# Kernel optimization log

Hardware: AMD Instinct MI355X
Metric: run time of the kernel (lower is better)

The kernel has to match this reference:

```python
import jax, jax.numpy as jnp
import numpy as np

N = 50000      # nodes
E = 800000     # edges (before self-loops)
H = 4          # heads
C = 64         # hidden_unit per head
IN = 256       # input_dim
OUT = 64       # output_dim
NEG = 0.2      # LeakyReLU slope in GATConv
EPS = 1e-5     # BatchNorm eps


def setup_inputs() -> dict:
    key = jax.random.key(0)
    ks = jax.random.split(key, 12)
    s = 0.05
    HC = H * C
    return {
        'x': jax.random.normal(ks[0], (N, IN), dtype=jnp.float32),
        'edge_index': jax.random.randint(ks[1], (2, E), 0, N, dtype=jnp.int64),
        # GATConv layer 1
        'W1': jax.random.normal(ks[2], (IN, HC), dtype=jnp.float32) * s,
        'att_src1': jax.random.normal(ks[3], (H, C), dtype=jnp.float32) * s,
        'att_dst1': jax.random.normal(ks[4], (H, C), dtype=jnp.float32) * s,
        'b1': jnp.zeros((HC,), jnp.float32),
        # GATConv layer 2
        'W2': jax.random.normal(ks[5], (HC, HC), dtype=jnp.float32) * s,
        'att_src2': jax.random.normal(ks[6], (H, C), dtype=jnp.float32) * s,
        'att_dst2': jax.random.normal(ks[7], (H, C), dtype=jnp.float32) * s,
        'b2': jnp.zeros((HC,), jnp.float32),
        # BatchNorms
        'g1': jnp.ones((HC,), jnp.float32), 'beta1': jnp.zeros((HC,), jnp.float32),
        'g2': jnp.ones((HC,), jnp.float32), 'beta2': jnp.zeros((HC,), jnp.float32),
        # final Linear
        'Wl': jax.random.normal(ks[8], (HC, OUT), dtype=jnp.float32) * s,
        'bl': jnp.zeros((OUT,), jnp.float32),
    }


def gat_layer(x, src, dst, W, a_src, a_dst, b):
    # x: [N, F_in] -> per-head features [N, H, C]
    xh = (x @ W).reshape(-1, H, C)
    alpha_src = jnp.einsum('nhc,hc->nh', xh, a_src)   # [N, H]
    alpha_dst = jnp.einsum('nhc,hc->nh', xh, a_dst)   # [N, H]
    e = jax.nn.leaky_relu(alpha_src[src] + alpha_dst[dst], NEG)  # [Etot, H]
    # segment softmax over edges grouped by destination node
    m = jax.ops.segment_max(e, dst, num_segments=N)              # [N, H]
    ex = jnp.exp(e - m[dst])
    den = jax.ops.segment_sum(ex, dst, num_segments=N)           # [N, H]
    alpha = ex / (den[dst] + 1e-16)                              # [Etot, H]
    # weighted scatter-add aggregation
    out = jax.ops.segment_sum(alpha[:, :, None] * xh[src], dst, num_segments=N)
    return out.reshape(-1, H * C) + b


def batchnorm(x, g, beta):
    mu = x.mean(axis=0)
    var = x.var(axis=0)
    return (x - mu) * jax.lax.rsqrt(var + EPS) * g + beta


def reference(x, edge_index, W1, att_src1, att_dst1, b1,
              W2, att_src2, att_dst2, b2, g1, beta1, g2, beta2, Wl, bl):
    # GATConv adds self-loops by default
    loops = jnp.arange(N, dtype=edge_index.dtype)
    src = jnp.concatenate([edge_index[0], loops])
    dst = jnp.concatenate([edge_index[1], loops])
    h = batchnorm(gat_layer(x, src, dst, W1, att_src1, att_dst1, b1), g1, beta1)
    # dropout is identity in eval mode
    h = batchnorm(gat_layer(h, src, dst, W2, att_src2, att_dst2, b2), g2, beta2)
    emb = h @ Wl + bl
    out = jax.nn.log_softmax(emb, axis=1)
    return (out, emb)
```

## Files before the change

### kernel.cpp

```cpp
#include <hip/hip_runtime.h>
#include <cstdint>

#define NNODES 50000
#define NEDGES 800000
#define ETOT   (NEDGES + NNODES)
#define HEADS 4
#define CH 64
#define HC 256
#define INDIM 256
#define OUTDIM 64
#define NEG_SLOPE 0.2f
#define BN_EPS 1e-5f
#define NB 128

typedef unsigned short u16;
typedef unsigned int u32;
typedef __attribute__((ext_vector_type(8))) short short8;
typedef __attribute__((ext_vector_type(8))) unsigned short ushort8v;
typedef __attribute__((ext_vector_type(4))) float floatx4;

__device__ inline float bf2f(u16 u) {
    union { unsigned int i; float f; } c;
    c.i = ((unsigned int)u) << 16;
    return c.f;
}
__device__ inline u16 f2bf(float f) {
    union { float f; unsigned int i; } c;
    c.f = f;
    unsigned int u = c.i + 0x7fff + ((c.i >> 16) & 1);
    return (u16)(u >> 16);
}
__device__ __host__ inline int pos256(int b) {
    int h = b >> 6, c = b & 63;
    return h * 64 + (c & 15) * 4 + (c >> 4);
}
__device__ inline void async16(u16* lds, const u16* g) {
    __builtin_amdgcn_global_load_lds(
        (const __attribute__((address_space(1))) unsigned int*)g,
        (__attribute__((address_space(3))) unsigned int*)lds,
        16, 0, 0);
}


__global__ void hist_kernel(const int* __restrict__ ei, int* __restrict__ cnt) {
    int t = blockIdx.x * blockDim.x + threadIdx.x;
    if (t >= ETOT) return;
    int d = (t < NEDGES) ? ei[NEDGES + t] : (t - NEDGES);
    atomicAdd(&cnt[d], 1);
}

__global__ void scan1_kernel(const int* __restrict__ cnt, int* __restrict__ row_off,
                             int* __restrict__ blockSums) {
    __shared__ int tsum[256];
    const int tid = threadIdx.x;
    const int base = blockIdx.x * 4096 + tid * 16;
    int local[16];
    int run = 0;
#pragma unroll
    for (int i = 0; i < 16; ++i) {
        int idx = base + i;
        int v = (idx < NNODES) ? cnt[idx] : 0;
        local[i] = run;
        run += v;
    }
    tsum[tid] = run;
    __syncthreads();
    for (int d = 1; d < 256; d <<= 1) {
        int v = (tid >= d) ? tsum[tid - d] : 0;
        __syncthreads();
        tsum[tid] += v;
        __syncthreads();
    }
    int excl = (tid == 0) ? 0 : tsum[tid - 1];
#pragma unroll
    for (int i = 0; i < 16; ++i) {
        int idx = base + i;
        if (idx < NNODES) row_off[idx] = excl + local[i];
    }
    if (tid == 0) blockSums[blockIdx.x] = tsum[255];
}

__global__ void scan2_kernel(int* __restrict__ row_off, const int* __restrict__ blockSums,
                             int* __restrict__ nxt) {
    __shared__ int sprefix;
    if (threadIdx.x == 0) {
        int p = 0;
        for (int b = 0; b < (int)blockIdx.x; ++b) p += blockSums[b];
        sprefix = p;
    }
    __syncthreads();
    int prefix = sprefix;
    int base = blockIdx.x * 4096 + threadIdx.x * 16;
#pragma unroll
    for (int i = 0; i < 16; ++i) {
        int idx = base + i;
        if (idx < NNODES) {
            int v = row_off[idx] + prefix;
            row_off[idx] = v;
            nxt[idx] = v;
        }
    }
    if (blockIdx.x == 0 && threadIdx.x == 0) row_off[NNODES] = ETOT;
}

__global__ void fill_csr_kernel(const int* __restrict__ ei, int* __restrict__ nxt,
                                int2* __restrict__ csr_pair) {
    int t = blockIdx.x * blockDim.x + threadIdx.x;
    if (t >= ETOT) return;
    int s, d;
    if (t < NEDGES) { s = ei[t]; d = ei[NEDGES + t]; }
    else            { s = d = t - NEDGES; }
    int pos = atomicAdd(&nxt[d], 1);
    csr_pair[pos] = make_int2(s, d);
}


__global__ void wcast_kernel(const float* __restrict__ W, u16* __restrict__ Wt,
                             int K, int Ncols) {
    int t = blockIdx.x * blockDim.x + threadIdx.x;
    if (t >= K * Ncols) return;
    int k = t / Ncols, n = t - k * Ncols;
    Wt[n * K + k] = f2bf(W[t]);
}


template <bool AF32>
__global__ __launch_bounds__(256)
void gemm_gat_kernel(const void* __restrict__ Ap, const u16* __restrict__ Bt,
                     const float* __restrict__ bias,
                     const float* __restrict__ att_s, const float* __restrict__ att_d,
                     u16* __restrict__ xhp, float* __restrict__ asrc,
                     float* __restrict__ adst, int M, int K) {
    __shared__ u16 As[128 * 32];
    __shared__ u16 Bs[128 * 32];
    const int tid = threadIdx.x;
    const int wave = tid >> 6, lane = tid & 63;
    const int q15 = lane & 15, quad = lane >> 4;
    const int rowBase = blockIdx.y * 128;
    const int colBase = blockIdx.x * 128;
    const int waveM = (wave >> 1) * 64, waveN = (wave & 1) * 64;
    const int head = blockIdx.x * 2 + (wave & 1);

    floatx4 acc[4][4];
    floatx4 zero = {0.f, 0.f, 0.f, 0.f};
#pragma unroll
    for (int i = 0; i < 4; ++i)
#pragma unroll
        for (int j = 0; j < 4; ++j) acc[i][j] = zero;

    for (int kt = 0; kt < K; kt += 32) {
        if constexpr (AF32) {
            const float* A32 = (const float*)Ap;
#pragma unroll
            for (int rnd = 0; rnd < 4; ++rnd) {
                int slot = rnd * 256 + tid;
                int r = slot >> 3, c4 = (slot & 7) * 4;
                int ar = rowBase + r; if (ar >= M) ar = M - 1;
                float4 fv = *(const float4*)&A32[(size_t)ar * K + kt + c4];
                ushort4 o;
                o.x = f2bf(fv.x); o.y = f2bf(fv.y); o.z = f2bf(fv.z); o.w = f2bf(fv.w);
                *(ushort4*)&As[r * 32 + c4] = o;
            }
#pragma unroll
            for (int q = 0; q < 2; ++q) {
                int e8 = (wave * 2 + q) * 64 + lane;
                int r = e8 >> 2, c = (e8 & 3) * 8;
                async16(&Bs[(wave * 2 + q) * 512], &Bt[(size_t)(colBase + r) * K + kt + c]);
            }
        } else {
            const u16* A16 = (const u16*)Ap;
#pragma unroll
            for (int q = 0; q < 2; ++q) {
                int e8 = (wave * 2 + q) * 64 + lane;
                int r = e8 >> 2, c = (e8 & 3) * 8;
                int ar = rowBase + r; if (ar >= M) ar = M - 1;
                async16(&As[(wave * 2 + q) * 512], &A16[(size_t)ar * K + kt + c]);
                async16(&Bs[(wave * 2 + q) * 512], &Bt[(size_t)(colBase + r) * K + kt + c]);
            }
        }
        __syncthreads();

        short8 af[4], bfr[4];
#pragma unroll
        for (int i = 0; i < 4; ++i)
            af[i] = *(const short8*)&As[(waveM + i * 16 + q15) * 32 + quad * 8];
#pragma unroll
        for (int j = 0; j < 4; ++j)
            bfr[j] = *(const short8*)&Bs[(waveN + j * 16 + q15) * 32 + quad * 8];
#pragma unroll
        for (int i = 0; i < 4; ++i)
#pragma unroll
            for (int j = 0; j < 4; ++j)
                acc[i][j] = __builtin_amdgcn_mfma_f32_16x16x32_bf16(af[i], bfr[j], acc[i][j], 0, 0, 0);
        __syncthreads();
    }

    float bv[4], atsv[4], atdv[4];
#pragma unroll
    for (int j = 0; j < 4; ++j) {
        int gcol = colBase + waveN + j * 16 + q15;
        bv[j] = bias ? bias[gcol] : 0.f;
        int hc = head * CH + j * 16 + q15;
        atsv[j] = att_s[hc];
        atdv[j] = att_d[hc];
    }
    const int pbase = head * 64 + q15 * 4;

#pragma unroll
    for (int i = 0; i < 4; ++i) {
#pragma unroll
        for (int rr = 0; rr < 4; ++rr) {
            int grow = rowBase + waveM + i * 16 + quad * 4 + rr;
            float v[4];
#pragma unroll
            for (int j = 0; j < 4; ++j) v[j] = acc[i][j][rr] + bv[j];
            float s = v[0] * atsv[0] + v[1] * atsv[1] + v[2] * atsv[2] + v[3] * atsv[3];
            float d = v[0] * atdv[0] + v[1] * atdv[1] + v[2] * atdv[2] + v[3] * atdv[3];
#pragma unroll
            for (int off = 1; off <= 8; off <<= 1) {
                s += __shfl_xor(s, off, 64);
                d += __shfl_xor(d, off, 64);
            }
            ushort4 o;
            o.x = f2bf(v[0]); o.y = f2bf(v[1]); o.z = f2bf(v[2]); o.w = f2bf(v[3]);
            if (grow < M) {
                *(ushort4*)&xhp[(size_t)grow * HC + pbase] = o;
                if (q15 == 0) {
                    asrc[grow * 4 + head] = s;
                    adst[grow * 4 + head] = d;
                }
            }
        }
    }
}


__global__ void wedge_kernel(const int2* __restrict__ csr_pair,
                             const float* __restrict__ asrc, const float* __restrict__ adst,
                             u16* __restrict__ w4b) {
    int e = blockIdx.x * blockDim.x + threadIdx.x;
    if (e >= ETOT) return;
    int2 pr = csr_pair[e];
    float4 a = *(const float4*)&asrc[pr.x * 4];
    float4 b = *(const float4*)&adst[pr.y * 4];
    ushort4 r;
    float v;
    v = a.x + b.x; v = v > 0.f ? v : NEG_SLOPE * v; r.x = f2bf(__expf(v));
    v = a.y + b.y; v = v > 0.f ? v : NEG_SLOPE * v; r.y = f2bf(__expf(v));
    v = a.z + b.z; v = v > 0.f ? v : NEG_SLOPE * v; r.z = f2bf(__expf(v));
    v = a.w + b.w; v = v > 0.f ? v : NEG_SLOPE * v; r.w = f2bf(__expf(v));
    *(ushort4*)&w4b[(size_t)e * 4] = r;
}


__global__ __launch_bounds__(256)
void aggregate_kernel(const int* __restrict__ row_off, const int2* __restrict__ csr_pair,
                      const u16* __restrict__ w4b, const u16* __restrict__ xhp,
                      const float* __restrict__ bias, u16* __restrict__ out) {
    const int g = threadIdx.x >> 6;
    const int lane = threadIdx.x & 63;
    const int d = blockIdx.x * 4 + g;
    const int h = lane >> 4;
    const int c16 = lane & 15;
    const int poff = h * 64 + c16 * 4;
    const int hsel = h & 2;
    const int hsh = (h & 1) * 16;
    const int start = row_off[d], end = row_off[d + 1];
    float a0 = 0.f, a1 = 0.f, a2 = 0.f, a3 = 0.f, den = 0.f;

    for (int base = start; base < end; base += 64) {
        const int cnt = min(64, end - base);
        int sv = 0;
        u32 wx = 0, wy = 0;
        if (lane < cnt) {
            int e = base + lane;
            sv = csr_pair[e].x;
            uint2 wq = *(const uint2*)&w4b[(size_t)e * 4];
            wx = wq.x; wy = wq.y;
        }
        int k = 0;
        for (; k + 3 < cnt; k += 4) {
            int s0 = __builtin_amdgcn_readlane(sv, k);
            int s1 = __builtin_amdgcn_readlane(sv, k + 1);
            int s2 = __builtin_amdgcn_readlane(sv, k + 2);
            int s3 = __builtin_amdgcn_readlane(sv, k + 3);
            u32 x0w = __builtin_amdgcn_readlane((int)wx, k), y0w = __builtin_amdgcn_readlane((int)wy, k);
            u32 x1w = __builtin_amdgcn_readlane((int)wx, k + 1), y1w = __builtin_amdgcn_readlane((int)wy, k + 1);
            u32 x2w = __builtin_amdgcn_readlane((int)wx, k + 2), y2w = __builtin_amdgcn_readlane((int)wy, k + 2);
            u32 x3w = __builtin_amdgcn_readlane((int)wx, k + 3), y3w = __builtin_amdgcn_readlane((int)wy, k + 3);
            ushort4 v0 = *(const ushort4*)&xhp[(size_t)s0 * HC + poff];
            ushort4 v1 = *(const ushort4*)&xhp[(size_t)s1 * HC + poff];
            ushort4 v2 = *(const ushort4*)&xhp[(size_t)s2 * HC + poff];
            ushort4 v3 = *(const ushort4*)&xhp[(size_t)s3 * HC + poff];
            float w0 = bf2f((u16)((hsel ? y0w : x0w) >> hsh));
            float w1 = bf2f((u16)((hsel ? y1w : x1w) >> hsh));
            float w2 = bf2f((u16)((hsel ? y2w : x2w) >> hsh));
            float w3 = bf2f((u16)((hsel ? y3w : x3w) >> hsh));
            den += (w0 + w1) + (w2 + w3);
            a0 += w0 * bf2f(v0.x) + w1 * bf2f(v1.x) + w2 * bf2f(v2.x) + w3 * bf2f(v3.x);
            a1 += w0 * bf2f(v0.y) + w1 * bf2f(v1.y) + w2 * bf2f(v2.y) + w3 * bf2f(v3.y);
            a2 += w0 * bf2f(v0.z) + w1 * bf2f(v1.z) + w2 * bf2f(v2.z) + w3 * bf2f(v3.z);
            a3 += w0 * bf2f(v0.w) + w1 * bf2f(v1.w) + w2 * bf2f(v2.w) + w3 * bf2f(v3.w);
        }
        for (; k < cnt; ++k) {
            int s0 = __builtin_amdgcn_readlane(sv, k);
            u32 x0w = __builtin_amdgcn_readlane((int)wx, k), y0w = __builtin_amdgcn_readlane((int)wy, k);
            ushort4 v0 = *(const ushort4*)&xhp[(size_t)s0 * HC + poff];
            float w0 = bf2f((u16)((hsel ? y0w : x0w) >> hsh));
            den += w0;
            a0 += w0 * bf2f(v0.x);
            a1 += w0 * bf2f(v0.y);
            a2 += w0 * bf2f(v0.z);
            a3 += w0 * bf2f(v0.w);
        }
    }
    float inv = 1.f / (den + 1e-16f);
    const int ch0 = h * 64 + c16;
    ushort4 o;
    o.x = f2bf(a0 * inv + bias[ch0 +  0]);
    o.y = f2bf(a1 * inv + bias[ch0 + 16]);
    o.z = f2bf(a2 * inv + bias[ch0 + 32]);
    o.w = f2bf(a3 * inv + bias[ch0 + 48]);
    *(ushort4*)&out[(size_t)d * HC + poff] = o;
}


__global__ __launch_bounds__(256)
void bn_stats_kernel(const u16* __restrict__ x, float* __restrict__ part) {
    const int tid = threadIdx.x;
    float s[8] = {}, s2[8] = {};
    const size_t total = (size_t)NNODES * HC;
    const size_t stride = (size_t)NB * 256 * 8;
    for (size_t f = ((size_t)blockIdx.x * 256 + tid) * 8; f < total; f += stride) {
        ushort8v v = *(const ushort8v*)&x[f];
#pragma unroll
        for (int i = 0; i < 8; ++i) {
            float t = bf2f(v[i]);
            s[i] += t;
            s2[i] += t * t;
        }
    }
#pragma unroll
    for (int i = 0; i < 8; ++i) {
        s[i] += __shfl_xor(s[i], 32, 64);
        s2[i] += __shfl_xor(s2[i], 32, 64);
    }
    __shared__ float red[4][512];
    const int wave = tid >> 6, lane = tid & 63;
    if (lane < 32) {
#pragma unroll
        for (int i = 0; i < 8; ++i) {
            red[wave][lane * 8 + i] = s[i];
            red[wave][256 + lane * 8 + i] = s2[i];
        }
    }
    __syncthreads();
    for (int j = tid; j < 512; j += 256)
        part[(size_t)blockIdx.x * 512 + j] = red[0][j] + red[1][j] + red[2][j] + red[3][j];
}


__global__ __launch_bounds__(256)
void fold_kernel(const float* __restrict__ W, const float* __restrict__ part,
                 const float* __restrict__ g, const float* __restrict__ beta,
                 const float* __restrict__ baseBias,
                 u16* __restrict__ Wt, float* __restrict__ biasOut, int Ncols) {
    __shared__ float sh[256];
    __shared__ float stat2[2];
    const int b = blockIdx.x;
    const int tid = threadIdx.x;
    if (b < 256) {
        const int p = pos256(b);
        const int wave = tid >> 6, lane = tid & 63;
        if (wave < 2) {
            int off = wave * 256;
            float v = part[(size_t)lane * 512 + off + p] + part[(size_t)(lane + 64) * 512 + off + p];
#pragma unroll
            for (int o = 1; o <= 32; o <<= 1) v += __shfl_xor(v, o, 64);
            if (lane == 0) stat2[wave] = v;
        }
        __syncthreads();
        float mu = stat2[0] * (1.f / NNODES);
        float var = stat2[1] * (1.f / NNODES) - mu * mu;
        float rg = rsqrtf(var + BN_EPS) * g[b];
        for (int n = tid; n < Ncols; n += 256)
            Wt[n * 256 + p] = f2bf(W[b * Ncols + n] * rg);
    } else {
        const int p = pos256(tid);
        float sum = 0.f, sq = 0.f;
        for (int k = 0; k < NB; ++k) {
            sum += part[(size_t)k * 512 + p];
            sq += part[(size_t)k * 512 + 256 + p];
        }
        float mu = sum * (1.f / NNODES);
        float var = sq * (1.f / NNODES) - mu * mu;
        float rg = rsqrtf(var + BN_EPS) * g[tid];
        sh[tid] = beta[tid] - mu * rg;
        __syncthreads();
        if (tid < Ncols) {
            float acc = baseBias ? baseBias[tid] : 0.f;
            for (int k = 0; k < 256; ++k) acc += sh[k] * W[k * Ncols + tid];
            biasOut[tid] = acc;
        }
    }
}


__global__ __launch_bounds__(256)
void final_ls_kernel(const u16* __restrict__ A, const u16* __restrict__ Bt,
                     const float* __restrict__ bias,
                     float* __restrict__ emb, float* __restrict__ out, int M) {
    __shared__ u16 As[128 * 32];
    __shared__ u16 Bs[64 * 32];
    const int tid = threadIdx.x;
    const int wave = tid >> 6, lane = tid & 63;
    const int q15 = lane & 15, quad = lane >> 4;
    const int rowBase = blockIdx.x * 128;

    floatx4 acc[2][4];
    floatx4 zero = {0.f, 0.f, 0.f, 0.f};
#pragma unroll
    for (int i = 0; i < 2; ++i)
#pragma unroll
        for (int j = 0; j < 4; ++j) acc[i][j] = zero;

    for (int kt = 0; kt < 256; kt += 32) {
#pragma unroll
        for (int rnd = 0; rnd < 2; ++rnd) {
            int slot = rnd * 256 + wave * 64 + lane;
            int r = slot >> 2;
            int c = (slot & 3) * 8;
            int ar = rowBase + r; if (ar >= M) ar = M - 1;
            async16(&As[(rnd * 256 + wave * 64) * 8], &A[(size_t)ar * 256 + kt + c]);
        }
        {
            int slot = wave * 64 + lane;
            int r = slot >> 2;
            int c = (slot & 3) * 8;
            async16(&Bs[(wave * 64) * 8], &Bt[(size_t)r * 256 + kt + c]);
        }
        __syncthreads();

        short8 af[2], bfr[4];
#pragma unroll
        for (int i = 0; i < 2; ++i)
            af[i] = *(const short8*)&As[(wave * 32 + i * 16 + q15) * 32 + quad * 8];
#pragma unroll
        for (int j = 0; j < 4; ++j)
            bfr[j] = *(const short8*)&Bs[(j * 16 + q15) * 32 + quad * 8];
#pragma unroll
        for (int i = 0; i < 2; ++i)
#pragma unroll
            for (int j = 0; j < 4; ++j)
                acc[i][j] = __builtin_amdgcn_mfma_f32_16x16x32_bf16(af[i], bfr[j], acc[i][j], 0, 0, 0);
        __syncthreads();
    }

#pragma unroll
    for (int i = 0; i < 2; ++i) {
#pragma unroll
        for (int rr = 0; rr < 4; ++rr) {
            float v[4];
#pragma unroll
            for (int j = 0; j < 4; ++j) v[j] = acc[i][j][rr] + bias[j * 16 + q15];
            float m = fmaxf(fmaxf(v[0], v[1]), fmaxf(v[2], v[3]));
#pragma unroll
            for (int off = 1; off <= 8; off <<= 1) m = fmaxf(m, __shfl_xor(m, off, 64));
            float s = __expf(v[0] - m) + __expf(v[1] - m) + __expf(v[2] - m) + __expf(v[3] - m);
#pragma unroll
            for (int off = 1; off <= 8; off <<= 1) s += __shfl_xor(s, off, 64);
            float ls = m + logf(s);
            int grow = rowBase + wave * 32 + i * 16 + quad * 4 + rr;
            if (grow < M) {
#pragma unroll
                for (int j = 0; j < 4; ++j) {
                    int col = j * 16 + q15;
                    emb[(size_t)grow * OUTDIM + col] = v[j];
                    out[(size_t)grow * OUTDIM + col] = v[j] - ls;
                }
            }
        }
    }
}


extern "C" void kernel_launch(void* const* d_in, const int* in_sizes, int n_in,
                              void* d_out, int out_size, void* d_ws, size_t ws_size,
                              hipStream_t stream) {
    const float* x   = (const float*)d_in[0];
    const int*   ei  = (const int*)d_in[1];
    const float* W1  = (const float*)d_in[2];
    const float* at_s1 = (const float*)d_in[3];
    const float* at_d1 = (const float*)d_in[4];
    const float* b1  = (const float*)d_in[5];
    const float* W2  = (const float*)d_in[6];
    const float* at_s2 = (const float*)d_in[7];
    const float* at_d2 = (const float*)d_in[8];
    const float* b2  = (const float*)d_in[9];
    const float* g1  = (const float*)d_in[10];
    const float* be1 = (const float*)d_in[11];
    const float* g2  = (const float*)d_in[12];
    const float* be2 = (const float*)d_in[13];
    const float* Wl  = (const float*)d_in[14];
    const float* bl  = (const float*)d_in[15];

    float* out = (float*)d_out;
    float* emb = out + (size_t)NNODES * OUTDIM;

    char* ws = (char*)d_ws;
    size_t off = 0;
    auto alloc = [&](size_t bytes) {
        void* p = ws + off;
        off += (bytes + 255) & ~(size_t)255;
        return p;
    };
    int*   cnt     = (int*)alloc((size_t)NNODES * 4);
    int*   row_off = (int*)alloc((size_t)(NNODES + 1) * 4);
    int*   nxt     = (int*)alloc((size_t)NNODES * 4);
    int*   bsums   = (int*)alloc(64 * 4);
    int2*  csr_pair= (int2*)alloc((size_t)ETOT * 8);
    u16*   w4b     = (u16*)alloc((size_t)ETOT * 4 * 2);
    float* asrc    = (float*)alloc((size_t)NNODES * 4 * 4);
    float* adst    = (float*)alloc((size_t)NNODES * 4 * 4);
    u16*   xhp     = (u16*)alloc((size_t)NNODES * HC * 2);
    u16*   ag_bf   = (u16*)alloc((size_t)NNODES * HC * 2);
    u16*   w1t     = (u16*)alloc((size_t)HC * INDIM * 2);
    u16*   w2t     = (u16*)alloc((size_t)HC * HC * 2);
    u16*   wlt     = (u16*)alloc((size_t)OUTDIM * HC * 2);
    float* part    = (float*)alloc((size_t)NB * 512 * 4);
    float* bias2   = (float*)alloc(HC * 4);
    float* blp     = (float*)alloc(OUTDIM * 4);

    const int scanBlocks = (NNODES + 4095) / 4096;
    const int eBlocks = (ETOT + 255) / 256;

    hipMemsetAsync(cnt, 0, (size_t)NNODES * 4, stream);
    hist_kernel<<<eBlocks, 256, 0, stream>>>(ei, cnt);
    scan1_kernel<<<scanBlocks, 256, 0, stream>>>(cnt, row_off, bsums);
    scan2_kernel<<<scanBlocks, 256, 0, stream>>>(row_off, bsums, nxt);
    fill_csr_kernel<<<eBlocks, 256, 0, stream>>>(ei, nxt, csr_pair);

    wcast_kernel<<<(INDIM * HC + 255) / 256, 256, 0, stream>>>(W1, w1t, INDIM, HC);

    dim3 gemmGrid(2, (NNODES + 127) / 128);

    gemm_gat_kernel<true><<<gemmGrid, 256, 0, stream>>>(x, w1t, nullptr, at_s1, at_d1,
                                                        xhp, asrc, adst, NNODES, INDIM);
    wedge_kernel<<<eBlocks, 256, 0, stream>>>(csr_pair, asrc, adst, w4b);
    aggregate_kernel<<<NNODES / 4, 256, 0, stream>>>(row_off, csr_pair, w4b, xhp, b1, ag_bf);
    bn_stats_kernel<<<NB, 256, 0, stream>>>(ag_bf, part);
    fold_kernel<<<257, 256, 0, stream>>>(W2, part, g1, be1, nullptr, w2t, bias2, HC);

    gemm_gat_kernel<false><<<gemmGrid, 256, 0, stream>>>(ag_bf, w2t, bias2, at_s2, at_d2,
                                                         xhp, asrc, adst, NNODES, HC);
    wedge_kernel<<<eBlocks, 256, 0, stream>>>(csr_pair, asrc, adst, w4b);
    aggregate_kernel<<<NNODES / 4, 256, 0, stream>>>(row_off, csr_pair, w4b, xhp, b2, ag_bf);
    bn_stats_kernel<<<NB, 256, 0, stream>>>(ag_bf, part);
    fold_kernel<<<257, 256, 0, stream>>>(Wl, part, g2, be2, bl, wlt, blp, OUTDIM);

    final_ls_kernel<<<(NNODES + 127) / 128, 256, 0, stream>>>(ag_bf, wlt, blp, emb, out, NNODES);
}
```

Before: 510.9 us.

## Fuse edge attention weight computation into aggregation and shrink CSR to source-only

Removes the separate wedge kernel that wrote per-edge exp weights to global memory, and instead computes LeakyReLU+exp in the aggregation kernel from gathered asrc and a per-destination adst load. The CSR array now stores only source indices (int instead of int2), and fill_csr processes four edges per thread with batched atomics. This cuts two kernel launches and the per-edge weight write/read traffic, at the cost of an extra random asrc gather inside aggregation.

```diff
diff --git a/kernel.cpp b/kernel.cpp
--- a/kernel.cpp
+++ b/kernel.cpp
@@ -103,15 +103,22 @@
     if (blockIdx.x == 0 && threadIdx.x == 0) row_off[NNODES] = ETOT;
 }
 
+#define FILL_S (ETOT / 4)
 __global__ void fill_csr_kernel(const int* __restrict__ ei, int* __restrict__ nxt,
-                                int2* __restrict__ csr_pair) {
+                                int* __restrict__ csr_src) {
     int t = blockIdx.x * blockDim.x + threadIdx.x;
-    if (t >= ETOT) return;
-    int s, d;
-    if (t < NEDGES) { s = ei[t]; d = ei[NEDGES + t]; }
-    else            { s = d = t - NEDGES; }
-    int pos = atomicAdd(&nxt[d], 1);
-    csr_pair[pos] = make_int2(s, d);
+    if (t >= FILL_S) return;
+    int s[4], d[4], p[4];
+#pragma unroll
+    for (int k = 0; k < 4; ++k) {
+        int e = t + k * FILL_S;
+        if (e < NEDGES) { s[k] = ei[e]; d[k] = ei[NEDGES + e]; }
+        else            { s[k] = d[k] = e - NEDGES; }
+    }
+#pragma unroll
+    for (int k = 0; k < 4; ++k) p[k] = atomicAdd(&nxt[d[k]], 1);
+#pragma unroll
+    for (int k = 0; k < 4; ++k) csr_src[p[k]] = s[k];
 }
 
 
@@ -235,28 +242,11 @@
 }
 
 
-__global__ void wedge_kernel(const int2* __restrict__ csr_pair,
-                             const float* __restrict__ asrc, const float* __restrict__ adst,
-                             u16* __restrict__ w4b) {
-    int e = blockIdx.x * blockDim.x + threadIdx.x;
-    if (e >= ETOT) return;
-    int2 pr = csr_pair[e];
-    float4 a = *(const float4*)&asrc[pr.x * 4];
-    float4 b = *(const float4*)&adst[pr.y * 4];
-    ushort4 r;
-    float v;
-    v = a.x + b.x; v = v > 0.f ? v : NEG_SLOPE * v; r.x = f2bf(__expf(v));
-    v = a.y + b.y; v = v > 0.f ? v : NEG_SLOPE * v; r.y = f2bf(__expf(v));
-    v = a.z + b.z; v = v > 0.f ? v : NEG_SLOPE * v; r.z = f2bf(__expf(v));
-    v = a.w + b.w; v = v > 0.f ? v : NEG_SLOPE * v; r.w = f2bf(__expf(v));
-    *(ushort4*)&w4b[(size_t)e * 4] = r;
-}
-
-
 __global__ __launch_bounds__(256)
-void aggregate_kernel(const int* __restrict__ row_off, const int2* __restrict__ csr_pair,
-                      const u16* __restrict__ w4b, const u16* __restrict__ xhp,
-                      const float* __restrict__ bias, u16* __restrict__ out) {
+void aggregate_kernel(const int* __restrict__ row_off, const int* __restrict__ csr_src,
+                      const float* __restrict__ asrc, const float* __restrict__ adst,
+                      const u16* __restrict__ xhp, const float* __restrict__ bias,
+                      u16* __restrict__ out) {
     const int g = threadIdx.x >> 6;
     const int lane = threadIdx.x & 63;
     const int d = blockIdx.x * 4 + g;
@@ -266,6 +256,7 @@
     const int hsel = h & 2;
     const int hsh = (h & 1) * 16;
     const int start = row_off[d], end = row_off[d + 1];
+    const float4 ad4 = *(const float4*)&adst[d * 4];
     float a0 = 0.f, a1 = 0.f, a2 = 0.f, a3 = 0.f, den = 0.f;
 
     for (int base = start; base < end; base += 64) {
@@ -273,10 +264,14 @@
         int sv = 0;
         u32 wx = 0, wy = 0;
         if (lane < cnt) {
-            int e = base + lane;
-            sv = csr_pair[e].x;
-            uint2 wq = *(const uint2*)&w4b[(size_t)e * 4];
-            wx = wq.x; wy = wq.y;
+            sv = csr_src[base + lane];
+            float4 as4 = *(const float4*)&asrc[sv * 4];
+            float e0 = as4.x + ad4.x; e0 = e0 > 0.f ? e0 : NEG_SLOPE * e0;
+            float e1 = as4.y + ad4.y; e1 = e1 > 0.f ? e1 : NEG_SLOPE * e1;
+            float e2 = as4.z + ad4.z; e2 = e2 > 0.f ? e2 : NEG_SLOPE * e2;
+            float e3 = as4.w + ad4.w; e3 = e3 > 0.f ? e3 : NEG_SLOPE * e3;
+            wx = (u32)f2bf(__expf(e0)) | ((u32)f2bf(__expf(e1)) << 16);
+            wy = (u32)f2bf(__expf(e2)) | ((u32)f2bf(__expf(e3)) << 16);
         }
         int k = 0;
         for (; k + 3 < cnt; k += 4) {
@@ -518,8 +513,7 @@
     int*   row_off = (int*)alloc((size_t)(NNODES + 1) * 4);
     int*   nxt     = (int*)alloc((size_t)NNODES * 4);
     int*   bsums   = (int*)alloc(64 * 4);
-    int2*  csr_pair= (int2*)alloc((size_t)ETOT * 8);
-    u16*   w4b     = (u16*)alloc((size_t)ETOT * 4 * 2);
+    int*   csr_src = (int*)alloc((size_t)ETOT * 4);
     float* asrc    = (float*)alloc((size_t)NNODES * 4 * 4);
     float* adst    = (float*)alloc((size_t)NNODES * 4 * 4);
     u16*   xhp     = (u16*)alloc((size_t)NNODES * HC * 2);
@@ -538,7 +532,7 @@
     hist_kernel<<<eBlocks, 256, 0, stream>>>(ei, cnt);
     scan1_kernel<<<scanBlocks, 256, 0, stream>>>(cnt, row_off, bsums);
     scan2_kernel<<<scanBlocks, 256, 0, stream>>>(row_off, bsums, nxt);
-    fill_csr_kernel<<<eBlocks, 256, 0, stream>>>(ei, nxt, csr_pair);
+    fill_csr_kernel<<<(FILL_S + 255) / 256, 256, 0, stream>>>(ei, nxt, csr_src);
 
     wcast_kernel<<<(INDIM * HC + 255) / 256, 256, 0, stream>>>(W1, w1t, INDIM, HC);
 
@@ -546,15 +540,13 @@
 
     gemm_gat_kernel<true><<<gemmGrid, 256, 0, stream>>>(x, w1t, nullptr, at_s1, at_d1,
                                                         xhp, asrc, adst, NNODES, INDIM);
-    wedge_kernel<<<eBlocks, 256, 0, stream>>>(csr_pair, asrc, adst, w4b);
-    aggregate_kernel<<<NNODES / 4, 256, 0, stream>>>(row_off, csr_pair, w4b, xhp, b1, ag_bf);
+    aggregate_kernel<<<NNODES / 4, 256, 0, stream>>>(row_off, csr_src, asrc, adst, xhp, b1, ag_bf);
     bn_stats_kernel<<<NB, 256, 0, stream>>>(ag_bf, part);
     fold_kernel<<<257, 256, 0, stream>>>(W2, part, g1, be1, nullptr, w2t, bias2, HC);
 
     gemm_gat_kernel<false><<<gemmGrid, 256, 0, stream>>>(ag_bf, w2t, bias2, at_s2, at_d2,
                                                          xhp, asrc, adst, NNODES, HC);
-    wedge_kernel<<<eBlocks, 256, 0, stream>>>(csr_pair, asrc, adst, w4b);
-    aggregate_kernel<<<NNODES / 4, 256, 0, stream>>>(row_off, csr_pair, w4b, xhp, b2, ag_bf);
+    aggregate_kernel<<<NNODES / 4, 256, 0, stream>>>(row_off, csr_src, asrc, adst, xhp, b2, ag_bf);
     bn_stats_kernel<<<NB, 256, 0, stream>>>(ag_bf, part);
     fold_kernel<<<257, 256, 0, stream>>>(Wl, part, g2, be2, bl, wlt, blp, OUTDIM);
 
```

After: 492.8 us. 3.5% less time.
